# Kernel tuning notes

Measured on AMD Instinct MI355X. Metric: run time of the kernel, lower is better.

## Reference

```python
import jax, jax.numpy as jnp
import numpy as np

B = 16384        # batch of states
D_IN = 512       # num_inputs (= num_gating_input)
H0 = 1024        # hidden_layer[0]
H1 = 1024        # hidden_layer[1]
D_OUT = 64       # num_outputs
E = 8            # num_experts (hard-coded in module)
G_H = 128        # gate MLP hidden width


def setup_inputs() -> dict:
    key = jax.random.key(0)
    ks = jax.random.split(key, 14)
    s = 0.05
    return {
        "inputs": jax.random.normal(ks[0], (B, D_IN), dtype=jnp.float32),
        # gate MLP: Linear(D_IN,128) -> relu -> Linear(128,128) -> relu -> Linear(128,E)
        "gw1": jax.random.normal(ks[1], (D_IN, G_H), dtype=jnp.float32) * s,
        "gb1": jnp.zeros((G_H,), dtype=jnp.float32),
        "gw2": jax.random.normal(ks[2], (G_H, G_H), dtype=jnp.float32) * s,
        "gb2": jnp.zeros((G_H,), dtype=jnp.float32),
        "gw3": jax.random.normal(ks[3], (G_H, E), dtype=jnp.float32) * s,
        "gb3": jnp.zeros((E,), dtype=jnp.float32),
        # expert (policy) layers: (weight [E,in,out], bias [E,1,out])
        "w0": jax.random.normal(ks[4], (E, D_IN, H0), dtype=jnp.float32) * s,
        "b0": jax.random.normal(ks[5], (E, 1, H0), dtype=jnp.float32) * s,
        "w1": jax.random.normal(ks[6], (E, H0, H1), dtype=jnp.float32) * s,
        "b1": jax.random.normal(ks[7], (E, 1, H1), dtype=jnp.float32) * s,
        "w2": jax.random.normal(ks[8], (E, H1, D_OUT), dtype=jnp.float32) * s,
        "b2": jax.random.normal(ks[9], (E, 1, D_OUT), dtype=jnp.float32) * s,
    }


def reference(inputs, gw1, gb1, gw2, gb2, gw3, gb3, w0, b0, w1, b1, w2, b2):
    # Gate: softmax over experts, torch code reshapes to [E, B, 1] via .t().unsqueeze(-1);
    # here keep g as [B, E] and contract the expert axis directly.
    h = jax.nn.relu(inputs @ gw1 + gb1)
    h = jax.nn.relu(h @ gw2 + gb2)
    g = jax.nn.softmax(h @ gw3 + gb3, axis=1)  # [B, E]

    def expert_layer(x, w, b, act):
        # out.matmul(weight) : [B,d] x [E,d,h] -> [E,B,h]; +bias; *gate; sum over E
        y = jnp.einsum('bd,edh->ebh', x, w) + b      # [E, B, h]
        return act(jnp.einsum('be,ebh->bh', g, y))   # [B, h]

    x = expert_layer(inputs, w0, b0, jax.nn.relu)
    x = expert_layer(x, w1, b1, jax.nn.relu)
    x = expert_layer(x, w2, b2, jnp.tanh)
    return x
```

## Files before the change

### kernel.cpp

```cpp
#include <hip/hip_runtime.h>
#include <hip/hip_bf16.h>
#include <cstdint>

#define DI __device__ __forceinline__

typedef unsigned short ushort_t;
using u16x8  = __attribute__((ext_vector_type(8))) unsigned short;
using bf16x8 = __attribute__((ext_vector_type(8))) __bf16;
using f32x4  = __attribute__((ext_vector_type(4))) float;

typedef const __attribute__((address_space(1))) void GVOID;
typedef __attribute__((address_space(3))) void LVOID;

enum { BB = 16384, DIN = 512, H0 = 1024, H1 = 1024, DOUT = 64, NE = 8, GH = 128 };

DI void async_ld16(const void* g, void* l) {
    __builtin_amdgcn_global_load_lds((GVOID*)g, (LVOID*)l, 16, 0, 0);
}

DI unsigned short f2bf(float f) {
    union { float f; unsigned u; } v; v.f = f;
    unsigned r = v.u + 0x7FFF + ((v.u >> 16) & 1);
    return (unsigned short)(r >> 16);
}
DI float bf2f(unsigned short u) { return __uint_as_float(((unsigned)u) << 16); }
DI f32x4 zero4() { f32x4 v = {0.f, 0.f, 0.f, 0.f}; return v; }

#define BARRIER() do { __builtin_amdgcn_s_barrier(); asm volatile("" ::: "memory"); } while (0)
#define LGKM0()   asm volatile("s_waitcnt lgkmcnt(0)" ::: "memory")

__global__ void f32_to_bf16_vec(const float* __restrict__ in, ushort_t* __restrict__ out) {
    const int i = (blockIdx.x * 256 + threadIdx.x) * 8;
    const float4 a = *(const float4*)&in[i];
    const float4 b = *(const float4*)&in[i + 4];
    u16x8 o;
    o[0] = f2bf(a.x); o[1] = f2bf(a.y); o[2] = f2bf(a.z); o[3] = f2bf(a.w);
    o[4] = f2bf(b.x); o[5] = f2bf(b.y); o[6] = f2bf(b.z); o[7] = f2bf(b.w);
    *(u16x8*)&out[i] = o;
}

__global__ void transpose_convert(const float* __restrict__ W, ushort_t* __restrict__ Wt,
                                  int K, int N, int Kext) {
    __shared__ float t[64][69];
    const int tid = threadIdx.x;
    const int k0 = blockIdx.x * 64, n0 = blockIdx.y * 64;
    for (int rr = tid >> 4; rr < 64; rr += 16) {
        const int c = (tid & 15) * 4;
        const float4 v = *(const float4*)&W[(size_t)(k0 + rr) * N + n0 + c];
        t[rr][c] = v.x; t[rr][c + 1] = v.y; t[rr][c + 2] = v.z; t[rr][c + 3] = v.w;
    }
    __syncthreads();
    for (int nn = tid >> 3; nn < 64; nn += 32) {
        const int k8 = (tid & 7) * 8;
        u16x8 o;
#pragma unroll
        for (int j = 0; j < 8; ++j) o[j] = f2bf(t[k8 + j][nn]);
        *(u16x8*)&Wt[(size_t)(n0 + nn) * Kext + k0 + k8] = o;
    }
}

__global__ void bias_fill(const float* __restrict__ bias, ushort_t* __restrict__ Wt,
                          int N, int K, int Kext) {
    const int n = blockIdx.x, c = threadIdx.x;
    Wt[(size_t)n * Kext + K + c] = (c < 8) ? f2bf(bias[(size_t)c * N + n]) : (ushort_t)0;
}

__global__ void gate3_softmax(const ushort_t* __restrict__ h2, const float* __restrict__ gw3,
                              const float* __restrict__ gb3, float* __restrict__ g,
                              ushort_t* __restrict__ Gx) {
    __shared__ float w[GH * NE];
    const int tid = threadIdx.x;
    for (int i = tid; i < GH * NE; i += 256) w[i] = gw3[i];
    __syncthreads();
    const int b = blockIdx.x * 256 + tid;
    float lg[NE];
#pragma unroll
    for (int e = 0; e < NE; ++e) lg[e] = gb3[e];
    const ushort_t* row = h2 + (size_t)b * GH;
    for (int h8 = 0; h8 < GH; h8 += 8) {
        const u16x8 v = *(const u16x8*)&row[h8];
#pragma unroll
        for (int j = 0; j < 8; ++j) {
            const float xv = bf2f(v[j]);
#pragma unroll
            for (int e = 0; e < NE; ++e) lg[e] += xv * w[(h8 + j) * NE + e];
        }
    }
    float mx = lg[0];
#pragma unroll
    for (int e = 1; e < NE; ++e) mx = fmaxf(mx, lg[e]);
    float s = 0.f;
#pragma unroll
    for (int e = 0; e < NE; ++e) { lg[e] = __expf(lg[e] - mx); s += lg[e]; }
    const float inv = 1.f / s;
#pragma unroll
    for (int e = 0; e < NE; ++e) g[(size_t)b * NE + e] = lg[e] * inv;
    ushort_t* gxr = Gx + (size_t)b * 128;
    u16x8 o;
#pragma unroll
    for (int e = 0; e < NE; ++e) o[e] = f2bf(lg[e] * inv);
    *(u16x8*)gxr = o;
    u16x8 z = {0, 0, 0, 0, 0, 0, 0, 0};
#pragma unroll
    for (int i = 1; i < 16; ++i) *(u16x8*)(gxr + i * 8) = z;
}

template <int TPE64, int STRIDEX>
__global__ __launch_bounds__(512, 2) void gemm256p(
    const ushort_t* __restrict__ X,
    const ushort_t* __restrict__ Gx,
    const ushort_t* __restrict__ Wt,
    const float* __restrict__ gvec,
    ushort_t* __restrict__ out,
    int N, int Kext) {
    constexpr int TE64 = NE * TPE64;
    const int NT = Kext >> 6;
    const int tid = threadIdx.x;
    const int wid = tid >> 6, l = tid & 63;
    const int wm = wid >> 2, wn = wid & 3;
    const int lr = l & 15, lk = l >> 4;

    const int b = blockIdx.x;
    const int xcd = b & 7, j2 = b >> 3;
    const int by = j2 & 3, bx = xcd + 8 * (j2 >> 2);
    const int bm0 = bx * 256, bn0 = by * 256;

    __shared__ __align__(1024) char lA[2][2][16384];
    __shared__ __align__(1024) char lB[2][2][16384];
    __shared__ float rtab[256 * 8];

    for (int r = tid; r < 256; r += 512) {
        const float* gr = gvec + (size_t)(bm0 + r) * 8;
        float ge[8];
#pragma unroll
        for (int e = 0; e < 8; ++e) ge[e] = gr[e];
#pragma unroll
        for (int e = 0; e < 7; ++e) rtab[r * 8 + e] = ge[e] / ge[e + 1];
        rtab[r * 8 + 7] = ge[7];
    }

    const int srow = (wid << 3) + (l >> 3);
    const int scol = (((l & 7) ^ (srow & 7)) << 3);
    auto stA = [&](int t, int h) {
        char* dst = (char*)lA[t & 1][h] + (wid << 10);
        if (t < TE64) {
            const ushort_t* s = X + (size_t)(bm0 + h * 128 + srow) * STRIDEX
                                  + (t & (TPE64 - 1)) * 64 + scol;
            async_ld16(s, dst);
            async_ld16(s + (size_t)64 * STRIDEX, dst + 8192);
        } else {
            const ushort_t* s = Gx + (size_t)(bm0 + h * 128 + srow) * 128
                                   + (t - TE64) * 64 + scol;
            async_ld16(s, dst);
            async_ld16(s + 64 * 128, dst + 8192);
        }
    };
    auto stB = [&](int t, int h) {
        char* dst = (char*)lB[t & 1][h] + (wid << 10);
        const ushort_t* s = Wt + (size_t)(bn0 + h * 128 + srow) * (size_t)Kext
                              + t * 64 + scol;
        async_ld16(s, dst);
        async_ld16(s + (size_t)64 * Kext, dst + 8192);
    };

    const int chunk0 = ((lk ^ (lr & 7)) << 4);
    const int aoff = lr * 128;
    const int boff = ((wn & 1) << 13) + lr * 128;

    f32x4 acc[8][4];
#pragma unroll
    for (int m = 0; m < 8; ++m)
#pragma unroll
        for (int n = 0; n < 4; ++n) acc[m][n] = zero4();

    stB(0, 0); stB(0, 1); stA(0, 0); stA(0, 1);
    stB(1, 0); stB(1, 1);
    LGKM0();
    asm volatile("s_waitcnt vmcnt(4)" ::: "memory");
    BARRIER();

    for (int t = 0; t < NT; ++t) {
        const char* Ah = (const char*)lA[t & 1][wm] + aoff;
        const char* Bh = (const char*)lB[t & 1][wn >> 1] + boff;
        bf16x8 a0[4], a1[4], b0[4], b1[4];

#pragma unroll
        for (int m = 0; m < 4; ++m) {
            a0[m] = *(const bf16x8*)(Ah + m * 2048 + chunk0);
            a1[m] = *(const bf16x8*)(Ah + m * 2048 + (chunk0 ^ 64));
        }
#pragma unroll
        for (int n = 0; n < 4; ++n) {
            b0[n] = *(const bf16x8*)(Bh + n * 2048 + chunk0);
            b1[n] = *(const bf16x8*)(Bh + n * 2048 + (chunk0 ^ 64));
        }
        if (t + 1 < NT) { stA(t + 1, 0); stA(t + 1, 1); }
        BARRIER();
        __builtin_amdgcn_s_setprio(1);
#pragma unroll
        for (int m = 0; m < 4; ++m)
#pragma unroll
            for (int n = 0; n < 4; ++n) {
                acc[m][n] = __builtin_amdgcn_mfma_f32_16x16x32_bf16(a0[m], b0[n], acc[m][n], 0, 0, 0);
                acc[m][n] = __builtin_amdgcn_mfma_f32_16x16x32_bf16(a1[m], b1[n], acc[m][n], 0, 0, 0);
            }
        __builtin_amdgcn_s_setprio(0);
        BARRIER();

#pragma unroll
        for (int m = 0; m < 4; ++m) {
            a0[m] = *(const bf16x8*)(Ah + (m + 4) * 2048 + chunk0);
            a1[m] = *(const bf16x8*)(Ah + (m + 4) * 2048 + (chunk0 ^ 64));
        }
        if (t + 2 < NT) { stB(t + 2, 0); stB(t + 2, 1); }
        BARRIER();
        __builtin_amdgcn_s_setprio(1);
#pragma unroll
        for (int m = 0; m < 4; ++m)
#pragma unroll
            for (int n = 0; n < 4; ++n) {
                acc[m + 4][n] = __builtin_amdgcn_mfma_f32_16x16x32_bf16(a0[m], b0[n], acc[m + 4][n], 0, 0, 0);
                acc[m + 4][n] = __builtin_amdgcn_mfma_f32_16x16x32_bf16(a1[m], b1[n], acc[m + 4][n], 0, 0, 0);
            }
        __builtin_amdgcn_s_setprio(0);

        if (t < TE64 && ((t + 1) & (TPE64 - 1)) == 0) {
            const int e = t / TPE64;
#pragma unroll
            for (int m = 0; m < 8; ++m)
#pragma unroll
                for (int q = 0; q < 4; ++q) {
                    const float r = rtab[(wm * 128 + m * 16 + lk * 4 + q) * 8 + e];
#pragma unroll
                    for (int n = 0; n < 4; ++n) acc[m][n][q] *= r;
                }
        }
        if (t + 2 < NT) {
            asm volatile("s_waitcnt vmcnt(4)" ::: "memory");
            BARRIER();
        } else if (t + 1 < NT) {
            asm volatile("s_waitcnt vmcnt(0)" ::: "memory");
            BARRIER();
        }
    }

#pragma unroll
    for (int m = 0; m < 8; ++m) {
        const int row = bm0 + wm * 128 + m * 16 + lk * 4;
#pragma unroll
        for (int n = 0; n < 4; ++n) {
            const int col = bn0 + wn * 64 + n * 16 + lr;
#pragma unroll
            for (int q = 0; q < 4; ++q) {
                const float v = fmaxf(acc[m][n][q], 0.f);
                out[(size_t)(row + q) * N + col] = f2bf(v);
            }
        }
    }
}

template <int BN, int TPE, int ACT, bool GATED, bool OUTF32>
__global__ __launch_bounds__(256, 2) void moe_gemm(
    const ushort_t* __restrict__ X, const ushort_t* __restrict__ Wt,
    const float* __restrict__ gvec, const float* __restrict__ bias,
    void* __restrict__ outv, int M, int N, int K, int Klen) {
    constexpr int BM = 128, BK = 64;
    constexpr int NF = BN / 32;
    const int tid = threadIdx.x;
    const int wid = tid >> 6, lane = tid & 63;
    const int lr = lane & 15, lk = lane >> 4;
    const int bm0 = blockIdx.x * BM;
    const int bn0 = blockIdx.y * BN;
    const int wm0 = (wid >> 1) * 64;
    const int wn0 = (wid & 1) * (BN / 2);
    const int koff = blockIdx.z * Klen;
    const int te0 = (TPE > 0) ? koff / (TPE * BK) : 0;

    __shared__ short lds_a[BM * BK];
    __shared__ short lds_b[BN * BK];
    __shared__ float lds_g[BM * 8];
    __shared__ float lds_bias[8 * BN];

    if constexpr (GATED) {
        ((f32x4*)lds_g)[tid] = ((const f32x4*)(gvec + (size_t)bm0 * 8))[tid];
        if constexpr (ACT != 2) {
            for (int i = tid; i < 8 * BN; i += 256) {
                const int e = i / BN, n = i - e * BN;
                lds_bias[i] = bias[(size_t)e * N + bn0 + n];
            }
        }
    }

    f32x4 acc_t[4][NF], acc_p[4][NF];
#pragma unroll
    for (int m = 0; m < 4; ++m)
#pragma unroll
        for (int n = 0; n < NF; ++n) { acc_t[m][n] = zero4(); acc_p[m][n] = zero4(); }

    f32x4(&amain)[4][NF] = GATED ? acc_p : acc_t;

    const int xstride = (TPE > 0) ? TPE * BK : K;
    const int NT = Klen / BK;
    for (int kt = 0; kt < NT; ++kt) {
        int kcolA;
        if constexpr (TPE > 0) kcolA = (kt % TPE) * BK; else kcolA = kt * BK;
        {
            const ushort_t* abase = X + (size_t)bm0 * xstride + kcolA;
#pragma unroll
            for (int c = wid; c < (BM * BK * 2) / 1024; c += 4) {
                const int off = c * 1024 + lane * 16;
                const int r = off >> 7, cbyte = off & 127;
                async_ld16((const char*)abase + (size_t)r * (xstride * 2) + cbyte,
                           (char*)lds_a + c * 1024);
            }
            const ushort_t* bbase = Wt + (size_t)bn0 * K + koff + kt * BK;
#pragma unroll
            for (int c = wid; c < (BN * BK * 2) / 1024; c += 4) {
                const int off = c * 1024 + lane * 16;
                const int r = off >> 7, cbyte = off & 127;
                async_ld16((const char*)bbase + (size_t)r * ((size_t)K * 2) + cbyte,
                           (char*)lds_b + c * 1024);
            }
        }
        __syncthreads();

        bf16x8 af[2][4], bfr[2][NF];
#pragma unroll
        for (int k2 = 0; k2 < 2; ++k2) {
#pragma unroll
            for (int m = 0; m < 4; ++m)
                af[k2][m] = *(const bf16x8*)&lds_a[(wm0 + m * 16 + lr) * BK + k2 * 32 + lk * 8];
#pragma unroll
            for (int n = 0; n < NF; ++n)
                bfr[k2][n] = *(const bf16x8*)&lds_b[(wn0 + n * 16 + lr) * BK + k2 * 32 + lk * 8];
        }
#pragma unroll
        for (int m = 0; m < 4; ++m)
#pragma unroll
            for (int n = 0; n < NF; ++n) {
                amain[m][n] = __builtin_amdgcn_mfma_f32_16x16x32_bf16(af[0][m], bfr[0][n], amain[m][n], 0, 0, 0);
                amain[m][n] = __builtin_amdgcn_mfma_f32_16x16x32_bf16(af[1][m], bfr[1][n], amain[m][n], 0, 0, 0);
            }

        if constexpr (TPE > 0 && GATED) {
            if ((kt + 1) % TPE == 0) {
                const int e = te0 + kt / TPE;
#pragma unroll
                for (int m = 0; m < 4; ++m)
#pragma unroll
                    for (int q = 0; q < 4; ++q) {
                        const float gw = lds_g[(wm0 + m * 16 + lk * 4 + q) * 8 + e];
#pragma unroll
                        for (int n = 0; n < NF; ++n) {
                            acc_t[m][n][q] += gw * acc_p[m][n][q];
                            acc_p[m][n][q] = 0.f;
                        }
                    }
            }
        }
        __syncthreads();
    }

#pragma unroll
    for (int m = 0; m < 4; ++m)
#pragma unroll
        for (int n = 0; n < NF; ++n)
#pragma unroll
            for (int q = 0; q < 4; ++q) {
                const int row = wm0 + m * 16 + lk * 4 + q;
                const int col = wn0 + n * 16 + lr;
                float v = acc_t[m][n][q];
                if constexpr (ACT != 2) {
                    if constexpr (GATED) {
                        float bs = 0.f;
#pragma unroll
                        for (int e = 0; e < 8; ++e) bs += lds_g[row * 8 + e] * lds_bias[e * BN + col];
                        v += bs;
                    } else {
                        v += bias[bn0 + col];
                    }
                }
                if constexpr (ACT == 0) v = fmaxf(v, 0.f);
                else if constexpr (ACT == 1) v = tanhf(v);
                const size_t oidx = (size_t)blockIdx.z * M * N + (size_t)(bm0 + row) * N + (bn0 + col);
                if constexpr (OUTF32) ((float*)outv)[oidx] = v;
                else ((ushort_t*)outv)[oidx] = f2bf(v);
            }
}

__global__ void splitk_reduce8(const float* __restrict__ part, const float* __restrict__ g,
                               const float* __restrict__ b2, float* __restrict__ out) {
    __shared__ float bs[8 * 64];
    const int tid = threadIdx.x;
    for (int i = tid; i < 512; i += 256) bs[i] = b2[i];
    __syncthreads();
    const int idx = blockIdx.x * 256 + tid;
    const int bb = idx >> 6, n = idx & 63;
    const float* gr = g + (size_t)bb * 8;
    float v = 0.f;
#pragma unroll
    for (int e = 0; e < 8; ++e)
        v += gr[e] * (part[(size_t)e * BB * 64 + idx] + bs[e * 64 + n]);
    out[idx] = tanhf(v);
}

extern "C" void kernel_launch(void* const* d_in, const int* in_sizes, int n_in,
                              void* d_out, int out_size, void* d_ws, size_t ws_size,
                              hipStream_t stream) {
    const float* inputs = (const float*)d_in[0];
    const float* gw1 = (const float*)d_in[1];
    const float* gb1 = (const float*)d_in[2];
    const float* gw2 = (const float*)d_in[3];
    const float* gb2 = (const float*)d_in[4];
    const float* gw3 = (const float*)d_in[5];
    const float* gb3 = (const float*)d_in[6];
    const float* w0 = (const float*)d_in[7];
    const float* b0 = (const float*)d_in[8];
    const float* w1 = (const float*)d_in[9];
    const float* b1 = (const float*)d_in[10];
    const float* w2 = (const float*)d_in[11];
    const float* b2 = (const float*)d_in[12];
    (void)in_sizes; (void)n_in; (void)out_size; (void)ws_size;

    constexpr int KE0 = NE * DIN + 128;
    constexpr int KE1 = NE * H0 + 128;

    char* ws = (char*)d_ws;
    ushort_t* x0b = (ushort_t*)(ws + 0);
    ushort_t* W0t = (ushort_t*)(ws + 16777216);
    ushort_t* G1t = (ushort_t*)(ws + 25427968);
    ushort_t* G2t = (ushort_t*)(ws + 25559040);
    ushort_t* h1b = (ushort_t*)(ws + 25591808);
    ushort_t* h2b = (ushort_t*)(ws + 29786112);
    ushort_t* x2b = (ushort_t*)(ws + 0);
    ushort_t* W1t = (ushort_t*)(ws + 33980416);
    ushort_t* W2t = (ushort_t*)(ws + 51019776);
    float*    gv  = (float*)(ws + 52068352);
    ushort_t* Gx  = (ushort_t*)(ws + 52592640);
    ushort_t* x1b = (ushort_t*)(ws + 56786944);
    float*    p2  = (float*)(ws + 56786944);

    f32_to_bf16_vec<<<dim3((BB * DIN) / (256 * 8)), 256, 0, stream>>>(inputs, x0b);
    transpose_convert<<<dim3((NE * DIN) / 64, H0 / 64), 256, 0, stream>>>(w0, W0t, NE * DIN, H0, KE0);
    transpose_convert<<<dim3((NE * H0) / 64, H1 / 64), 256, 0, stream>>>(w1, W1t, NE * H0, H1, KE1);
    transpose_convert<<<dim3((NE * H1) / 64, DOUT / 64), 256, 0, stream>>>(w2, W2t, NE * H1, DOUT, NE * H1);
    transpose_convert<<<dim3(DIN / 64, GH / 64), 256, 0, stream>>>(gw1, G1t, DIN, GH, DIN);
    transpose_convert<<<dim3(GH / 64, GH / 64), 256, 0, stream>>>(gw2, G2t, GH, GH, GH);
    bias_fill<<<dim3(H0), 128, 0, stream>>>(b0, W0t, H0, NE * DIN, KE0);
    bias_fill<<<dim3(H1), 128, 0, stream>>>(b1, W1t, H1, NE * H0, KE1);

    moe_gemm<64, 0, 0, false, false><<<dim3(BB / 128, GH / 64), 256, 0, stream>>>(
        x0b, G1t, nullptr, gb1, h1b, BB, GH, DIN, DIN);
    moe_gemm<64, 0, 0, false, false><<<dim3(BB / 128, GH / 64), 256, 0, stream>>>(
        h1b, G2t, nullptr, gb2, h2b, BB, GH, GH, GH);
    gate3_softmax<<<dim3(BB / 256), 256, 0, stream>>>(h2b, gw3, gb3, gv, Gx);

    gemm256p<DIN / 64, DIN><<<dim3((BB / 256) * (H0 / 256)), 512, 0, stream>>>(
        x0b, Gx, W0t, gv, x1b, H0, KE0);
    gemm256p<H0 / 64, H0><<<dim3((BB / 256) * (H1 / 256)), 512, 0, stream>>>(
        x1b, Gx, W1t, gv, x2b, H1, KE1);

    moe_gemm<64, 16, 2, false, true><<<dim3(BB / 128, DOUT / 64, 8), 256, 0, stream>>>(
        x2b, W2t, nullptr, nullptr, p2, BB, DOUT, NE * H1, H1);
    splitk_reduce8<<<dim3((BB * DOUT) / 256), 256, 0, stream>>>(p2, gv, b2, (float*)d_out);
}
```

Before: 438.4 us.

## Replace 256x256 LDS-staged GEMM with 128x128 tile loading A directly to registers

Swaps the main expert GEMM for a 128x128 tile, 4-wave kernel that stages only the weight operand B through double-buffered LDS and loads the activation operand A straight from global memory into registers each k-step. It also drops the hand-tuned vmcnt waits, split barriers and setprio scheduling in favour of a single __syncthreads per iteration. The aim is to cut LDS traffic and shared memory footprint. In exchange, each wave re-reads the A tile from global/L2 with strided accesses, data reuse per tile is lower, and global load latency is no longer hidden by async prefetch.

Result: slower. 1.699 ms (+287.6%).

```diff
diff --git a/kernel.cpp b/kernel.cpp
--- a/kernel.cpp
+++ b/kernel.cpp
@@ -25,9 +25,6 @@
 }
 DI float bf2f(unsigned short u) { return __uint_as_float(((unsigned)u) << 16); }
 DI f32x4 zero4() { f32x4 v = {0.f, 0.f, 0.f, 0.f}; return v; }
-
-#define BARRIER() do { __builtin_amdgcn_s_barrier(); asm volatile("" ::: "memory"); } while (0)
-#define LGKM0()   asm volatile("s_waitcnt lgkmcnt(0)" ::: "memory")
 
 __global__ void f32_to_bf16_vec(const float* __restrict__ in, ushort_t* __restrict__ out) {
     const int i = (blockIdx.x * 256 + threadIdx.x) * 8;
@@ -106,7 +103,7 @@
 }
 
 template <int TPE64, int STRIDEX>
-__global__ __launch_bounds__(512, 2) void gemm256p(
+__global__ __launch_bounds__(256, 2) void gemm_areg(
     const ushort_t* __restrict__ X,
     const ushort_t* __restrict__ Gx,
     const ushort_t* __restrict__ Wt,
@@ -117,112 +114,85 @@
     const int NT = Kext >> 6;
     const int tid = threadIdx.x;
     const int wid = tid >> 6, l = tid & 63;
-    const int wm = wid >> 2, wn = wid & 3;
+    const int wn = wid;
     const int lr = l & 15, lk = l >> 4;
 
     const int b = blockIdx.x;
-    const int xcd = b & 7, j2 = b >> 3;
-    const int by = j2 & 3, bx = xcd + 8 * (j2 >> 2);
-    const int bm0 = bx * 256, bn0 = by * 256;
-
-    __shared__ __align__(1024) char lA[2][2][16384];
-    __shared__ __align__(1024) char lB[2][2][16384];
-    __shared__ float rtab[256 * 8];
-
-    for (int r = tid; r < 256; r += 512) {
-        const float* gr = gvec + (size_t)(bm0 + r) * 8;
+    const int xcd = b & 7;
+    const int by = (b >> 3) & 7;
+    const int bx = xcd + 8 * (b >> 6);
+    const int bm0 = bx * 128, bn0 = by * 128;
+
+    __shared__ __align__(1024) char lB[2][16384];
+    __shared__ float rtab[128 * 8];
+
+    if (tid < 128) {
+        const float* gr = gvec + (size_t)(bm0 + tid) * 8;
         float ge[8];
 #pragma unroll
         for (int e = 0; e < 8; ++e) ge[e] = gr[e];
 #pragma unroll
-        for (int e = 0; e < 7; ++e) rtab[r * 8 + e] = ge[e] / ge[e + 1];
-        rtab[r * 8 + 7] = ge[7];
-    }
-
-    const int srow = (wid << 3) + (l >> 3);
-    const int scol = (((l & 7) ^ (srow & 7)) << 3);
-    auto stA = [&](int t, int h) {
-        char* dst = (char*)lA[t & 1][h] + (wid << 10);
+        for (int e = 0; e < 7; ++e) rtab[tid * 8 + e] = ge[e] / ge[e + 1];
+        rtab[tid * 8 + 7] = ge[7];
+    }
+
+    auto stB = [&](int t, int buf) {
+#pragma unroll
+        for (int r = 0; r < 4; ++r) {
+            char* dst = (char*)lB[buf] + r * 4096 + (wid << 10);
+            const int row = r * 32 + wid * 8 + (l >> 3);
+            const int col = t * 64 + (((l & 7) ^ ((l >> 3) & 7)) << 3);
+            async_ld16(Wt + (size_t)(bn0 + row) * Kext + col, dst);
+        }
+    };
+
+    const int bc0 = ((lk ^ (lr & 7)) << 4);
+    const int boff = (wn * 32 + lr) * 128;
+
+    const ushort_t* aX = X + (size_t)(bm0 + lr) * STRIDEX + lk * 8;
+    const ushort_t* aG = Gx + (size_t)(bm0 + lr) * 128 + lk * 8;
+
+    f32x4 acc[8][2];
+#pragma unroll
+    for (int m = 0; m < 8; ++m) { acc[m][0] = zero4(); acc[m][1] = zero4(); }
+
+    stB(0, 0);
+    __syncthreads();
+
+    int buf = 0;
+    for (int t = 0; t < NT; ++t) {
+        if (t + 1 < NT) stB(t + 1, buf ^ 1);
+
+        const char* Bp = lB[buf];
+        bf16x8 b00, b01, b10, b11;
+        b00 = *(const bf16x8*)(Bp + boff + bc0);
+        b01 = *(const bf16x8*)(Bp + boff + (bc0 ^ 64));
+        b10 = *(const bf16x8*)(Bp + boff + 2048 + bc0);
+        b11 = *(const bf16x8*)(Bp + boff + 2048 + (bc0 ^ 64));
+
         if (t < TE64) {
-            const ushort_t* s = X + (size_t)(bm0 + h * 128 + srow) * STRIDEX
-                                  + (t & (TPE64 - 1)) * 64 + scol;
-            async_ld16(s, dst);
-            async_ld16(s + (size_t)64 * STRIDEX, dst + 8192);
+            const ushort_t* ap = aX + (t & (TPE64 - 1)) * 64;
+#pragma unroll
+            for (int m = 0; m < 8; ++m) {
+                const bf16x8 a0 = *(const bf16x8*)(ap + (size_t)(m * 16) * STRIDEX);
+                const bf16x8 a1 = *(const bf16x8*)(ap + (size_t)(m * 16) * STRIDEX + 32);
+                acc[m][0] = __builtin_amdgcn_mfma_f32_16x16x32_bf16(a0, b00, acc[m][0], 0, 0, 0);
+                acc[m][0] = __builtin_amdgcn_mfma_f32_16x16x32_bf16(a1, b01, acc[m][0], 0, 0, 0);
+                acc[m][1] = __builtin_amdgcn_mfma_f32_16x16x32_bf16(a0, b10, acc[m][1], 0, 0, 0);
+                acc[m][1] = __builtin_amdgcn_mfma_f32_16x16x32_bf16(a1, b11, acc[m][1], 0, 0, 0);
+            }
         } else {
-            const ushort_t* s = Gx + (size_t)(bm0 + h * 128 + srow) * 128
-                                   + (t - TE64) * 64 + scol;
-            async_ld16(s, dst);
-            async_ld16(s + 64 * 128, dst + 8192);
-        }
-    };
-    auto stB = [&](int t, int h) {
-        char* dst = (char*)lB[t & 1][h] + (wid << 10);
-        const ushort_t* s = Wt + (size_t)(bn0 + h * 128 + srow) * (size_t)Kext
-                              + t * 64 + scol;
-        async_ld16(s, dst);
-        async_ld16(s + (size_t)64 * Kext, dst + 8192);
-    };
-
-    const int chunk0 = ((lk ^ (lr & 7)) << 4);
-    const int aoff = lr * 128;
-    const int boff = ((wn & 1) << 13) + lr * 128;
-
-    f32x4 acc[8][4];
-#pragma unroll
-    for (int m = 0; m < 8; ++m)
-#pragma unroll
-        for (int n = 0; n < 4; ++n) acc[m][n] = zero4();
-
-    stB(0, 0); stB(0, 1); stA(0, 0); stA(0, 1);
-    stB(1, 0); stB(1, 1);
-    LGKM0();
-    asm volatile("s_waitcnt vmcnt(4)" ::: "memory");
-    BARRIER();
-
-    for (int t = 0; t < NT; ++t) {
-        const char* Ah = (const char*)lA[t & 1][wm] + aoff;
-        const char* Bh = (const char*)lB[t & 1][wn >> 1] + boff;
-        bf16x8 a0[4], a1[4], b0[4], b1[4];
-
-#pragma unroll
-        for (int m = 0; m < 4; ++m) {
-            a0[m] = *(const bf16x8*)(Ah + m * 2048 + chunk0);
-            a1[m] = *(const bf16x8*)(Ah + m * 2048 + (chunk0 ^ 64));
-        }
-#pragma unroll
-        for (int n = 0; n < 4; ++n) {
-            b0[n] = *(const bf16x8*)(Bh + n * 2048 + chunk0);
-            b1[n] = *(const bf16x8*)(Bh + n * 2048 + (chunk0 ^ 64));
-        }
-        if (t + 1 < NT) { stA(t + 1, 0); stA(t + 1, 1); }
-        BARRIER();
-        __builtin_amdgcn_s_setprio(1);
-#pragma unroll
-        for (int m = 0; m < 4; ++m)
-#pragma unroll
-            for (int n = 0; n < 4; ++n) {
-                acc[m][n] = __builtin_amdgcn_mfma_f32_16x16x32_bf16(a0[m], b0[n], acc[m][n], 0, 0, 0);
-                acc[m][n] = __builtin_amdgcn_mfma_f32_16x16x32_bf16(a1[m], b1[n], acc[m][n], 0, 0, 0);
-            }
-        __builtin_amdgcn_s_setprio(0);
-        BARRIER();
-
-#pragma unroll
-        for (int m = 0; m < 4; ++m) {
-            a0[m] = *(const bf16x8*)(Ah + (m + 4) * 2048 + chunk0);
-            a1[m] = *(const bf16x8*)(Ah + (m + 4) * 2048 + (chunk0 ^ 64));
-        }
-        if (t + 2 < NT) { stB(t + 2, 0); stB(t + 2, 1); }
-        BARRIER();
-        __builtin_amdgcn_s_setprio(1);
-#pragma unroll
-        for (int m = 0; m < 4; ++m)
-#pragma unroll
-            for (int n = 0; n < 4; ++n) {
-                acc[m + 4][n] = __builtin_amdgcn_mfma_f32_16x16x32_bf16(a0[m], b0[n], acc[m + 4][n], 0, 0, 0);
-                acc[m + 4][n] = __builtin_amdgcn_mfma_f32_16x16x32_bf16(a1[m], b1[n], acc[m + 4][n], 0, 0, 0);
-            }
-        __builtin_amdgcn_s_setprio(0);
+            const ushort_t* ap = aG + (t - TE64) * 64;
+#pragma unroll
+            for (int m = 0; m < 8; ++m) {
+                const bf16x8 a0 = *(const bf16x8*)(ap + (size_t)(m * 16) * 128);
+                const bf16x8 a1 = *(const bf16x8*)(ap + (size_t)(m * 16) * 128 + 32);
+                acc[m][0] = __builtin_amdgcn_mfma_f32_16x16x32_bf16(a0, b00, acc[m][0], 0, 0, 0);
+                acc[m][0] = __builtin_amdgcn_mfma_f32_16x16x32_bf16(a1, b01, acc[m][0], 0, 0, 0);
+                acc[m][1] = __builtin_amdgcn_mfma_f32_16x16x32_bf16(a0, b10, acc[m][1], 0, 0, 0);
+                acc[m][1] = __builtin_amdgcn_mfma_f32_16x16x32_bf16(a1, b11, acc[m][1], 0, 0, 0);
+            }
+        }
 
         if (t < TE64 && ((t + 1) & (TPE64 - 1)) == 0) {
             const int e = t / TPE64;
@@ -230,26 +200,22 @@
             for (int m = 0; m < 8; ++m)
 #pragma unroll
                 for (int q = 0; q < 4; ++q) {
-                    const float r = rtab[(wm * 128 + m * 16 + lk * 4 + q) * 8 + e];
-#pragma unroll
-                    for (int n = 0; n < 4; ++n) acc[m][n][q] *= r;
+                    const float r = rtab[(m * 16 + lk * 4 + q) * 8 + e];
+                    acc[m][0][q] *= r;
+                    acc[m][1][q] *= r;
                 }
         }
-        if (t + 2 < NT) {
-            asm volatile("s_waitcnt vmcnt(4)" ::: "memory");
-            BARRIER();
-        } else if (t + 1 < NT) {
-            asm volatile("s_waitcnt vmcnt(0)" ::: "memory");
-            BARRIER();
-        }
+
+        buf ^= 1;
+        __syncthreads();
     }
 
 #pragma unroll
     for (int m = 0; m < 8; ++m) {
-        const int row = bm0 + wm * 128 + m * 16 + lk * 4;
-#pragma unroll
-        for (int n = 0; n < 4; ++n) {
-            const int col = bn0 + wn * 64 + n * 16 + lr;
+        const int row = bm0 + m * 16 + lk * 4;
+#pragma unroll
+        for (int n = 0; n < 2; ++n) {
+            const int col = bn0 + wn * 32 + n * 16 + lr;
 #pragma unroll
             for (int q = 0; q < 4; ++q) {
                 const float v = fmaxf(acc[m][n][q], 0.f);
@@ -455,9 +421,9 @@
         h1b, G2t, nullptr, gb2, h2b, BB, GH, GH, GH);
     gate3_softmax<<<dim3(BB / 256), 256, 0, stream>>>(h2b, gw3, gb3, gv, Gx);
 
-    gemm256p<DIN / 64, DIN><<<dim3((BB / 256) * (H0 / 256)), 512, 0, stream>>>(
+    gemm_areg<DIN / 64, DIN><<<dim3((BB / 128) * (H0 / 128)), 256, 0, stream>>>(
         x0b, Gx, W0t, gv, x1b, H0, KE0);
-    gemm256p<H0 / 64, H0><<<dim3((BB / 256) * (H1 / 256)), 512, 0, stream>>>(
+    gemm_areg<H0 / 64, H0><<<dim3((BB / 128) * (H1 / 128)), 256, 0, stream>>>(
         x1b, Gx, W1t, gv, x2b, H1, KE1);
 
     moe_gemm<64, 16, 2, false, true><<<dim3(BB / 128, DOUT / 64, 8), 256, 0, stream>>>(
```
